# Kernel optimization log

Measured on AMD Instinct MI355X. Metric: run time of the kernel, lower is better.

The kernel has to match this reference:

```python
import jax, jax.numpy as jnp
import numpy as np

EMBED_SIZE = 100
HEAD_SIZE = 64
B, T = 4, 4096


def setup_inputs() -> dict:
    key = jax.random.key(0)
    k1, k2, k3, k4 = jax.random.split(key, 4)
    x = jax.random.normal(k1, (B, T, EMBED_SIZE), dtype=jnp.float32)
    Wq = jax.random.normal(k2, (EMBED_SIZE, HEAD_SIZE), dtype=jnp.float32) * 0.1
    Wk = jax.random.normal(k3, (EMBED_SIZE, HEAD_SIZE), dtype=jnp.float32) * 0.1
    Wv = jax.random.normal(k4, (EMBED_SIZE, HEAD_SIZE), dtype=jnp.float32) * 0.1
    return {"x": x, "Wq": Wq, "Wk": Wk, "Wv": Wv}


def reference(x, Wq, Wk, Wv):
    # Projections (bias-free Linear): [B, T, head_size]
    q = x @ Wq
    k = x @ Wk
    v = x @ Wv
    scale = HEAD_SIZE ** (-0.5)
    # Scaled scores [B, T, T]
    scores = jnp.einsum("bqd,bkd->bqk", q, k) * scale
    # Faithful to source: tril the scores, then mask entries that equal 0 to -inf
    masked = jnp.tril(scores)
    masked = jnp.where(masked == 0, -jnp.inf, masked)
    attn = jax.nn.softmax(masked, axis=-1)
    out = jnp.einsum("bqk,bkd->bqd", attn, v)  # [B, T, head_size]
    return out
```

## Files before the change

kernel.cpp:

```cpp
#include <hip/hip_runtime.h>
#include <hip/hip_bf16.h>
#include <stdint.h>

#define NB 4
#define NT 4096
#define NE 100
#define ND 64

typedef __attribute__((ext_vector_type(8))) short short8;
typedef __attribute__((ext_vector_type(4))) short short4_;
typedef __attribute__((ext_vector_type(4))) float float4_;
typedef unsigned short ushort_t;

__device__ __forceinline__ unsigned short f2bf(float f) {
  union { float f; uint32_t u; } v; v.f = f;
  uint32_t u = v.u;
  u += 0x7fffu + ((u >> 16) & 1u);
  return (unsigned short)(u >> 16);
}

__device__ __forceinline__ float bf2f(short us) {
  union { uint32_t u; float f; } v;
  v.u = ((uint32_t)(unsigned short)us) << 16;
  return v.f;
}

__device__ __forceinline__ float fast_exp2(float x) {
#if __has_builtin(__builtin_amdgcn_exp2f)
  return __builtin_amdgcn_exp2f(x);
#else
  return exp2f(x);
#endif
}

__global__ __launch_bounds__(256) void proj_kernel(
    const float* __restrict__ x, const float* __restrict__ Wq,
    const float* __restrict__ Wk, const float* __restrict__ Wv,
    ushort_t* __restrict__ Qb, ushort_t* __restrict__ Kb,
    ushort_t* __restrict__ Vt) {
  __shared__ __align__(16) float xs[16 * NE];
  __shared__ __align__(16) ushort_t Wl[3][25][64][4];
  ushort_t (*Vl)[72] = (ushort_t(*)[72])xs;

  const int tid = threadIdx.x;
  const int r0  = blockIdx.x * 16;

  {
    const float4_* xsrc = (const float4_*)(x + (size_t)r0 * NE);
    float4_* xdst = (float4_*)xs;
    #pragma unroll
    for (int i = tid; i < 400; i += 256) xdst[i] = xsrc[i];
  }
  {
    const int ch = tid >> 6, d = tid & 63;
    if (ch < 3) {
      const float* Ws = (ch == 0) ? Wq : (ch == 1) ? Wk : Wv;
      #pragma unroll 5
      for (int qd = 0; qd < 25; ++qd) {
        short4_ pk;
        #pragma unroll
        for (int jj = 0; jj < 4; ++jj)
          pk[jj] = (short)f2bf(Ws[(4*qd + jj)*ND + d]);
        *(short4_*)&Wl[ch][qd][d][0] = pk;
      }
    }
  }
  __syncthreads();

  const int wv = tid >> 6, lane = tid & 63;
  float aq[4] = {0,0,0,0}, ak[4] = {0,0,0,0}, av[4] = {0,0,0,0};
  const float* xw = xs + (wv * 4) * NE;

  for (int qd = 0; qd < 25; ++qd) {
    short4_ w4q = *(const short4_*)&Wl[0][qd][lane][0];
    short4_ w4k = *(const short4_*)&Wl[1][qd][lane][0];
    short4_ w4v = *(const short4_*)&Wl[2][qd][lane][0];
    float4_ x0 = *(const float4_*)&xw[0*NE + 4*qd];
    float4_ x1 = *(const float4_*)&xw[1*NE + 4*qd];
    float4_ x2 = *(const float4_*)&xw[2*NE + 4*qd];
    float4_ x3 = *(const float4_*)&xw[3*NE + 4*qd];
    #pragma unroll
    for (int jj = 0; jj < 4; ++jj) {
      float fq = bf2f(w4q[jj]), fk = bf2f(w4k[jj]), fv = bf2f(w4v[jj]);
      aq[0] += x0[jj]*fq; ak[0] += x0[jj]*fk; av[0] += x0[jj]*fv;
      aq[1] += x1[jj]*fq; ak[1] += x1[jj]*fk; av[1] += x1[jj]*fv;
      aq[2] += x2[jj]*fq; ak[2] += x2[jj]*fk; av[2] += x2[jj]*fv;
      aq[3] += x3[jj]*fq; ak[3] += x3[jj]*fk; av[3] += x3[jj]*fv;
    }
  }

  __syncthreads();

  const float QS = 0.125f * 1.44269504088896340736f;
  #pragma unroll
  for (int j = 0; j < 4; ++j) {
    int row = r0 + wv*4 + j;
    Qb[(size_t)row*ND + lane] = f2bf(aq[j] * QS);
    Kb[(size_t)row*ND + lane] = f2bf(ak[j]);
    Vl[wv*4 + j][lane] = f2bf(av[j]);
  }
  __syncthreads();

  if (tid < 128) {
    int d = tid >> 1, halfi = tid & 1;
    short8 pk;
    #pragma unroll
    for (int k2 = 0; k2 < 8; ++k2) pk[k2] = (short)Vl[halfi*8 + k2][d];
    int b = r0 >> 12, tg = (r0 & (NT-1)) + halfi*8;
    *(short8*)(Vt + ((size_t)(b*ND + d))*NT + tg) = pk;
  }
}

__global__ __launch_bounds__(128) void attn_kernel(
    const ushort_t* __restrict__ Qb,
    const ushort_t* __restrict__ Kb,
    const ushort_t* __restrict__ Vt,
    float* __restrict__ out) {
  __shared__ __align__(16) ushort_t Ks[2][64*64];
  __shared__ __align__(16) ushort_t Vs[2][64*64];
  __shared__ __align__(16) ushort_t Pbuf[2][16][72];

  const int tid  = threadIdx.x;
  const int w    = tid >> 6, lane = tid & 63;
  const int qrow = lane & 15, grp = lane >> 4;
  const int blk  = blockIdx.x;
  const int b    = blk >> 6;
  const int pr   = blk & 63;
  const int srow8 = lane >> 3, sc16 = lane & 7;

  const ushort_t* Kbase = Kb + (size_t)b*NT*ND;
  const ushort_t* Vtb   = Vt + (size_t)b*ND*NT;

  for (int half = 0; half < 2; ++half) {
    const int g  = half ? pr : (127 - pr);
    const int q0 = g << 5;
    const int nt = (g >> 1) + 1;
    const int qglob = q0 + 16*w + qrow;

    const ushort_t* Qr = Qb + ((size_t)(b*NT + q0 + 16*w + qrow))*ND + 8*grp;
    const short8 qf0 = *(const short8*)(Qr);
    const short8 qf1 = *(const short8*)(Qr + 32);

    float4_ O0 = {0,0,0,0}, O1 = {0,0,0,0}, O2 = {0,0,0,0}, O3 = {0,0,0,0};
    float m = -1e30f, lsum = 0.f;
    short8 sr[8];

    #pragma unroll
    for (int i = 0; i < 8; ++i) {
      int row = 8*i + srow8;
      sr[i] = (w == 0)
        ? *(const short8*)(Kbase + (size_t)row*ND + sc16*8)
        : *(const short8*)(Vtb + (size_t)row*NT + sc16*8);
    }
    {
      ushort_t* dst = (w == 0) ? Ks[0] : Vs[0];
      #pragma unroll
      for (int i = 0; i < 8; ++i) {
        int row = 8*i + srow8;
        *(short8*)&dst[row*64 + ((sc16 ^ (row & 7)) << 3)] = sr[i];
      }
    }
    __syncthreads();

    for (int t = 0; t < nt; ++t) {
      const int cur = t & 1;
      const int kv0 = t << 6;

      if (t + 1 < nt) {
        const int kn0 = kv0 + 64;
        #pragma unroll
        for (int i = 0; i < 8; ++i) {
          int row = 8*i + srow8;
          sr[i] = (w == 0)
            ? *(const short8*)(Kbase + (size_t)(kn0 + row)*ND + sc16*8)
            : *(const short8*)(Vtb + (size_t)row*NT + kn0 + sc16*8);
        }
      }

      const ushort_t* Kc = Ks[cur];
      const ushort_t* Vc = Vs[cur];

      float4_ s[4];
      #pragma unroll
      for (int st = 0; st < 4; ++st) {
        int row = st*16 + qrow;
        short8 kf0 = *(const short8*)&Kc[row*64 + (((grp    ) ^ (row & 7)) << 3)];
        short8 kf1 = *(const short8*)&Kc[row*64 + (((grp + 4) ^ (row & 7)) << 3)];
        float4_ acc = {0,0,0,0};
        acc = __builtin_amdgcn_mfma_f32_16x16x32_bf16(kf0, qf0, acc, 0,0,0);
        acc = __builtin_amdgcn_mfma_f32_16x16x32_bf16(kf1, qf1, acc, 0,0,0);
        s[st] = acc;
      }

      short8 vf[8];
      #pragma unroll
      for (int j = 0; j < 4; ++j) {
        int row = j*16 + qrow;
        vf[2*j]   = *(const short8*)&Vc[row*64 + (((grp    ) ^ (row & 7)) << 3)];
        vf[2*j+1] = *(const short8*)&Vc[row*64 + (((grp + 4) ^ (row & 7)) << 3)];
      }

      if (t == nt - 1) {
        #pragma unroll
        for (int st = 0; st < 4; ++st)
          #pragma unroll
          for (int r = 0; r < 4; ++r) {
            int kv = kv0 + st*16 + grp*4 + r;
            if (kv > qglob) s[st][r] = -1e30f;
          }
      }

      float pmax = s[0][0];
      #pragma unroll
      for (int st = 0; st < 4; ++st)
        #pragma unroll
        for (int r = 0; r < 4; ++r) pmax = fmaxf(pmax, s[st][r]);
      if (!__all(pmax <= m + 8.0f)) {
        float tm = pmax;
        tm = fmaxf(tm, __shfl_xor(tm, 16));
        tm = fmaxf(tm, __shfl_xor(tm, 32));
        const float mnew  = fmaxf(m, tm);
        const float alpha = fast_exp2(m - mnew);
        m = mnew;
        lsum *= alpha;
        #pragma unroll
        for (int r = 0; r < 4; ++r) {
          float ar = __shfl(alpha, grp*4 + r);
          O0[r] *= ar; O1[r] *= ar; O2[r] *= ar; O3[r] *= ar;
        }
      }

      float psum = 0.f;
      #pragma unroll
      for (int st = 0; st < 4; ++st) {
        short4_ pv;
        #pragma unroll
        for (int r = 0; r < 4; ++r) {
          float p = fast_exp2(s[st][r] - m);
          psum += p;
          pv[r] = (short)f2bf(p);
        }
        *(short4_*)&Pbuf[w][qrow][st*16 + grp*4] = pv;
      }
      psum += __shfl_xor(psum, 16);
      psum += __shfl_xor(psum, 32);
      lsum += psum;

      asm volatile("s_waitcnt lgkmcnt(0)" ::: "memory");

      const short8 pf0 = *(const short8*)&Pbuf[w][qrow][8*grp];
      const short8 pf1 = *(const short8*)&Pbuf[w][qrow][32 + 8*grp];
      O0 = __builtin_amdgcn_mfma_f32_16x16x32_bf16(pf0, vf[0], O0, 0,0,0);
      O0 = __builtin_amdgcn_mfma_f32_16x16x32_bf16(pf1, vf[1], O0, 0,0,0);
      O1 = __builtin_amdgcn_mfma_f32_16x16x32_bf16(pf0, vf[2], O1, 0,0,0);
      O1 = __builtin_amdgcn_mfma_f32_16x16x32_bf16(pf1, vf[3], O1, 0,0,0);
      O2 = __builtin_amdgcn_mfma_f32_16x16x32_bf16(pf0, vf[4], O2, 0,0,0);
      O2 = __builtin_amdgcn_mfma_f32_16x16x32_bf16(pf1, vf[5], O2, 0,0,0);
      O3 = __builtin_amdgcn_mfma_f32_16x16x32_bf16(pf0, vf[6], O3, 0,0,0);
      O3 = __builtin_amdgcn_mfma_f32_16x16x32_bf16(pf1, vf[7], O3, 0,0,0);

      if (t + 1 < nt) {
        ushort_t* dst = (w == 0) ? Ks[cur ^ 1] : Vs[cur ^ 1];
        #pragma unroll
        for (int i = 0; i < 8; ++i) {
          int row = 8*i + srow8;
          *(short8*)&dst[row*64 + ((sc16 ^ (row & 7)) << 3)] = sr[i];
        }
      }
      __syncthreads();
    }

    float* orow = out + ((size_t)(b*NT + q0 + 16*w)) * ND;
    #pragma unroll
    for (int r = 0; r < 4; ++r) {
      float ls  = __shfl(lsum, grp*4 + r);
      float inv = 1.f / ls;
      int qr = grp*4 + r;
      orow[qr*ND + 0*16 + qrow] = O0[r]*inv;
      orow[qr*ND + 1*16 + qrow] = O1[r]*inv;
      orow[qr*ND + 2*16 + qrow] = O2[r]*inv;
      orow[qr*ND + 3*16 + qrow] = O3[r]*inv;
    }
  }
}

extern "C" void kernel_launch(void* const* d_in, const int* in_sizes, int n_in,
                              void* d_out, int out_size, void* d_ws, size_t ws_size,
                              hipStream_t stream) {
  const float* x  = (const float*)d_in[0];
  const float* Wq = (const float*)d_in[1];
  const float* Wk = (const float*)d_in[2];
  const float* Wv = (const float*)d_in[3];
  float* out = (float*)d_out;

  ushort_t* Qb = (ushort_t*)d_ws;
  ushort_t* Kb = Qb + (size_t)NB*NT*ND;
  ushort_t* Vt = Kb + (size_t)NB*NT*ND;

  proj_kernel<<<dim3(1024), dim3(256), 0, stream>>>(x, Wq, Wk, Wv, Qb, Kb, Vt);
  attn_kernel<<<dim3(NB*64), dim3(128), 0, stream>>>(Qb, Kb, Vt, out);
}
```

Measured before the change: 144.0 us.

## Split long causal rows across KV blocks with last-block merge

The attention kernel now uses split-KV (flash-decoding style). Each query group is divided into up to four KV chunks according to its causal length, giving 1280 workgroups instead of 256. Partial O, m and l are written to workspace, and the last finishing block, found through an atomic counter, merges them. The projection kernel now handles 64 rows per block and zeroes the counters, with V transposed in its own shared buffer. This targets poor occupancy and the load imbalance of pairing rows, at the cost of partial-result traffic and a serial merge step.

```diff
diff --git a/kernel.cpp b/kernel.cpp
--- a/kernel.cpp
+++ b/kernel.cpp
@@ -37,19 +37,20 @@
     const float* __restrict__ x, const float* __restrict__ Wq,
     const float* __restrict__ Wk, const float* __restrict__ Wv,
     ushort_t* __restrict__ Qb, ushort_t* __restrict__ Kb,
-    ushort_t* __restrict__ Vt) {
-  __shared__ __align__(16) float xs[16 * NE];
+    ushort_t* __restrict__ Vt, int* __restrict__ cnt) {
+  __shared__ __align__(16) float xs[64 * NE];
   __shared__ __align__(16) ushort_t Wl[3][25][64][4];
-  ushort_t (*Vl)[72] = (ushort_t(*)[72])xs;
+  __shared__ __align__(16) ushort_t Vl[64][72];
 
   const int tid = threadIdx.x;
-  const int r0  = blockIdx.x * 16;
+  const int r0  = blockIdx.x * 64;
+
+  if (blockIdx.x == 0) { cnt[tid] = 0; cnt[tid + 256] = 0; }
 
   {
     const float4_* xsrc = (const float4_*)(x + (size_t)r0 * NE);
     float4_* xdst = (float4_*)xs;
-    #pragma unroll
-    for (int i = tid; i < 400; i += 256) xdst[i] = xsrc[i];
+    for (int i = tid; i < 1600; i += 256) xdst[i] = xsrc[i];
   }
   {
     const int ch = tid >> 6, d = tid & 63;
@@ -68,92 +69,210 @@
   __syncthreads();
 
   const int wv = tid >> 6, lane = tid & 63;
-  float aq[4] = {0,0,0,0}, ak[4] = {0,0,0,0}, av[4] = {0,0,0,0};
-  const float* xw = xs + (wv * 4) * NE;
-
-  for (int qd = 0; qd < 25; ++qd) {
-    short4_ w4q = *(const short4_*)&Wl[0][qd][lane][0];
-    short4_ w4k = *(const short4_*)&Wl[1][qd][lane][0];
-    short4_ w4v = *(const short4_*)&Wl[2][qd][lane][0];
-    float4_ x0 = *(const float4_*)&xw[0*NE + 4*qd];
-    float4_ x1 = *(const float4_*)&xw[1*NE + 4*qd];
-    float4_ x2 = *(const float4_*)&xw[2*NE + 4*qd];
-    float4_ x3 = *(const float4_*)&xw[3*NE + 4*qd];
-    #pragma unroll
-    for (int jj = 0; jj < 4; ++jj) {
-      float fq = bf2f(w4q[jj]), fk = bf2f(w4k[jj]), fv = bf2f(w4v[jj]);
-      aq[0] += x0[jj]*fq; ak[0] += x0[jj]*fk; av[0] += x0[jj]*fv;
-      aq[1] += x1[jj]*fq; ak[1] += x1[jj]*fk; av[1] += x1[jj]*fv;
-      aq[2] += x2[jj]*fq; ak[2] += x2[jj]*fk; av[2] += x2[jj]*fv;
-      aq[3] += x3[jj]*fq; ak[3] += x3[jj]*fk; av[3] += x3[jj]*fv;
-    }
-  }
-
+  const float QS = 0.125f * 1.44269504088896340736f;
+
+  for (int it = 0; it < 4; ++it) {
+    float aq[4] = {0,0,0,0}, ak[4] = {0,0,0,0}, av[4] = {0,0,0,0};
+    const float* xw = xs + (it*16 + wv*4) * NE;
+    for (int qd = 0; qd < 25; ++qd) {
+      short4_ w4q = *(const short4_*)&Wl[0][qd][lane][0];
+      short4_ w4k = *(const short4_*)&Wl[1][qd][lane][0];
+      short4_ w4v = *(const short4_*)&Wl[2][qd][lane][0];
+      float4_ x0 = *(const float4_*)&xw[0*NE + 4*qd];
+      float4_ x1 = *(const float4_*)&xw[1*NE + 4*qd];
+      float4_ x2 = *(const float4_*)&xw[2*NE + 4*qd];
+      float4_ x3 = *(const float4_*)&xw[3*NE + 4*qd];
+      #pragma unroll
+      for (int jj = 0; jj < 4; ++jj) {
+        float fq = bf2f(w4q[jj]), fk = bf2f(w4k[jj]), fv = bf2f(w4v[jj]);
+        aq[0] += x0[jj]*fq; ak[0] += x0[jj]*fk; av[0] += x0[jj]*fv;
+        aq[1] += x1[jj]*fq; ak[1] += x1[jj]*fk; av[1] += x1[jj]*fv;
+        aq[2] += x2[jj]*fq; ak[2] += x2[jj]*fk; av[2] += x2[jj]*fv;
+        aq[3] += x3[jj]*fq; ak[3] += x3[jj]*fk; av[3] += x3[jj]*fv;
+      }
+    }
+    #pragma unroll
+    for (int j = 0; j < 4; ++j) {
+      int lrow = it*16 + wv*4 + j;
+      int row  = r0 + lrow;
+      Qb[(size_t)row*ND + lane] = f2bf(aq[j] * QS);
+      Kb[(size_t)row*ND + lane] = f2bf(ak[j]);
+      Vl[lrow][lane] = f2bf(av[j]);
+    }
+  }
   __syncthreads();
 
-  const float QS = 0.125f * 1.44269504088896340736f;
-  #pragma unroll
-  for (int j = 0; j < 4; ++j) {
-    int row = r0 + wv*4 + j;
-    Qb[(size_t)row*ND + lane] = f2bf(aq[j] * QS);
-    Kb[(size_t)row*ND + lane] = f2bf(ak[j]);
-    Vl[wv*4 + j][lane] = f2bf(av[j]);
-  }
-  __syncthreads();
-
-  if (tid < 128) {
-    int d = tid >> 1, halfi = tid & 1;
-    short8 pk;
-    #pragma unroll
-    for (int k2 = 0; k2 < 8; ++k2) pk[k2] = (short)Vl[halfi*8 + k2][d];
-    int b = r0 >> 12, tg = (r0 & (NT-1)) + halfi*8;
-    *(short8*)(Vt + ((size_t)(b*ND + d))*NT + tg) = pk;
+  {
+    const int b = r0 >> 12, r0t = r0 & (NT - 1);
+    for (int i = tid; i < 512; i += 256) {
+      int d = i >> 3, seg = i & 7;
+      short8 pk;
+      #pragma unroll
+      for (int k2 = 0; k2 < 8; ++k2) pk[k2] = (short)Vl[seg*8 + k2][d];
+      *(short8*)(Vt + ((size_t)(b*ND + d))*NT + r0t + seg*8) = pk;
+    }
   }
 }
 
 __global__ __launch_bounds__(128) void attn_kernel(
-    const ushort_t* __restrict__ Qb,
-    const ushort_t* __restrict__ Kb,
-    const ushort_t* __restrict__ Vt,
+    const ushort_t* __restrict__ Qb, const ushort_t* __restrict__ Kb,
+    const ushort_t* __restrict__ Vt, float* __restrict__ part,
+    float* __restrict__ mlbuf, int* __restrict__ cnt,
     float* __restrict__ out) {
   __shared__ __align__(16) ushort_t Ks[2][64*64];
   __shared__ __align__(16) ushort_t Vs[2][64*64];
   __shared__ __align__(16) ushort_t Pbuf[2][16][72];
+  __shared__ int isLast;
 
   const int tid  = threadIdx.x;
   const int w    = tid >> 6, lane = tid & 63;
   const int qrow = lane & 15, grp = lane >> 4;
-  const int blk  = blockIdx.x;
-  const int b    = blk >> 6;
-  const int pr   = blk & 63;
   const int srow8 = lane >> 3, sc16 = lane & 7;
+
+  const int wid = blockIdx.x;
+  const int b   = wid / 320;
+  const int u   = 319 - (wid - b*320);
+  int g, s;
+  if (u < 32)       { g = u;                                s = 0; }
+  else if (u < 96)  { int v = u - 32;              g = 32 + (v >> 1); s = v & 1; }
+  else if (u < 192) { int v = u - 96; int q3 = v/3; g = 64 + q3;      s = v - 3*q3; }
+  else              { int v = u - 192;             g = 96 + (v >> 2); s = v & 3; }
+
+  const int nt = (g >> 1) + 1;
+  const int nw = (g + 32) >> 5;
+  const int t0 = s << 4;
+  const int t1 = min(nt, t0 + 16);
+  const int q0 = g << 5;
+  const int qglob = q0 + 16*w + qrow;
 
   const ushort_t* Kbase = Kb + (size_t)b*NT*ND;
   const ushort_t* Vtb   = Vt + (size_t)b*ND*NT;
 
-  for (int half = 0; half < 2; ++half) {
-    const int g  = half ? pr : (127 - pr);
-    const int q0 = g << 5;
-    const int nt = (g >> 1) + 1;
-    const int qglob = q0 + 16*w + qrow;
-
-    const ushort_t* Qr = Qb + ((size_t)(b*NT + q0 + 16*w + qrow))*ND + 8*grp;
-    const short8 qf0 = *(const short8*)(Qr);
-    const short8 qf1 = *(const short8*)(Qr + 32);
-
-    float4_ O0 = {0,0,0,0}, O1 = {0,0,0,0}, O2 = {0,0,0,0}, O3 = {0,0,0,0};
-    float m = -1e30f, lsum = 0.f;
-    short8 sr[8];
-
+  const ushort_t* Qr = Qb + ((size_t)(b*NT + q0 + 16*w + qrow))*ND + 8*grp;
+  const short8 qf0 = *(const short8*)(Qr);
+  const short8 qf1 = *(const short8*)(Qr + 32);
+
+  float4_ O0 = {0,0,0,0}, O1 = {0,0,0,0}, O2 = {0,0,0,0}, O3 = {0,0,0,0};
+  float m = -1e30f, lsum = 0.f;
+  short8 sr[8];
+
+  {
+    const int kv0 = t0 << 6;
     #pragma unroll
     for (int i = 0; i < 8; ++i) {
       int row = 8*i + srow8;
       sr[i] = (w == 0)
-        ? *(const short8*)(Kbase + (size_t)row*ND + sc16*8)
-        : *(const short8*)(Vtb + (size_t)row*NT + sc16*8);
-    }
-    {
-      ushort_t* dst = (w == 0) ? Ks[0] : Vs[0];
+        ? *(const short8*)(Kbase + (size_t)(kv0 + row)*ND + sc16*8)
+        : *(const short8*)(Vtb + (size_t)row*NT + kv0 + sc16*8);
+    }
+    ushort_t* dst = (w == 0) ? Ks[0] : Vs[0];
+    #pragma unroll
+    for (int i = 0; i < 8; ++i) {
+      int row = 8*i + srow8;
+      *(short8*)&dst[row*64 + ((sc16 ^ (row & 7)) << 3)] = sr[i];
+    }
+  }
+  __syncthreads();
+
+  for (int t = t0; t < t1; ++t) {
+    const int cur = (t - t0) & 1;
+    const int kv0 = t << 6;
+
+    if (t + 1 < t1) {
+      const int kn0 = kv0 + 64;
+      #pragma unroll
+      for (int i = 0; i < 8; ++i) {
+        int row = 8*i + srow8;
+        sr[i] = (w == 0)
+          ? *(const short8*)(Kbase + (size_t)(kn0 + row)*ND + sc16*8)
+          : *(const short8*)(Vtb + (size_t)row*NT + kn0 + sc16*8);
+      }
+    }
+
+    const ushort_t* Kc = Ks[cur];
+    const ushort_t* Vc = Vs[cur];
+
+    float4_ sA[4];
+    #pragma unroll
+    for (int st = 0; st < 4; ++st) {
+      int row = st*16 + qrow;
+      short8 kf0 = *(const short8*)&Kc[row*64 + (((grp    ) ^ (row & 7)) << 3)];
+      short8 kf1 = *(const short8*)&Kc[row*64 + (((grp + 4) ^ (row & 7)) << 3)];
+      float4_ acc = {0,0,0,0};
+      acc = __builtin_amdgcn_mfma_f32_16x16x32_bf16(kf0, qf0, acc, 0,0,0);
+      acc = __builtin_amdgcn_mfma_f32_16x16x32_bf16(kf1, qf1, acc, 0,0,0);
+      sA[st] = acc;
+    }
+
+    short8 vf[8];
+    #pragma unroll
+    for (int j = 0; j < 4; ++j) {
+      int row = j*16 + qrow;
+      vf[2*j]   = *(const short8*)&Vc[row*64 + (((grp    ) ^ (row & 7)) << 3)];
+      vf[2*j+1] = *(const short8*)&Vc[row*64 + (((grp + 4) ^ (row & 7)) << 3)];
+    }
+
+    if (t == nt - 1) {
+      #pragma unroll
+      for (int st = 0; st < 4; ++st)
+        #pragma unroll
+        for (int r = 0; r < 4; ++r) {
+          int kv = kv0 + st*16 + grp*4 + r;
+          if (kv > qglob) sA[st][r] = -1e30f;
+        }
+    }
+
+    float pmax = sA[0][0];
+    #pragma unroll
+    for (int st = 0; st < 4; ++st)
+      #pragma unroll
+      for (int r = 0; r < 4; ++r) pmax = fmaxf(pmax, sA[st][r]);
+    if (!__all(pmax <= m + 8.0f)) {
+      float tm = pmax;
+      tm = fmaxf(tm, __shfl_xor(tm, 16));
+      tm = fmaxf(tm, __shfl_xor(tm, 32));
+      const float mnew  = fmaxf(m, tm);
+      const float alpha = fast_exp2(m - mnew);
+      m = mnew;
+      lsum *= alpha;
+      #pragma unroll
+      for (int r = 0; r < 4; ++r) {
+        float ar = __shfl(alpha, grp*4 + r);
+        O0[r] *= ar; O1[r] *= ar; O2[r] *= ar; O3[r] *= ar;
+      }
+    }
+
+    float psum = 0.f;
+    #pragma unroll
+    for (int st = 0; st < 4; ++st) {
+      short4_ pv;
+      #pragma unroll
+      for (int r = 0; r < 4; ++r) {
+        float p = fast_exp2(sA[st][r] - m);
+        psum += p;
+        pv[r] = (short)f2bf(p);
+      }
+      *(short4_*)&Pbuf[w][qrow][st*16 + grp*4] = pv;
+    }
+    psum += __shfl_xor(psum, 16);
+    psum += __shfl_xor(psum, 32);
+    lsum += psum;
+
+    asm volatile("s_waitcnt lgkmcnt(0)" ::: "memory");
+
+    const short8 pf0 = *(const short8*)&Pbuf[w][qrow][8*grp];
+    const short8 pf1 = *(const short8*)&Pbuf[w][qrow][32 + 8*grp];
+    O0 = __builtin_amdgcn_mfma_f32_16x16x32_bf16(pf0, vf[0], O0, 0,0,0);
+    O0 = __builtin_amdgcn_mfma_f32_16x16x32_bf16(pf1, vf[1], O0, 0,0,0);
+    O1 = __builtin_amdgcn_mfma_f32_16x16x32_bf16(pf0, vf[2], O1, 0,0,0);
+    O1 = __builtin_amdgcn_mfma_f32_16x16x32_bf16(pf1, vf[3], O1, 0,0,0);
+    O2 = __builtin_amdgcn_mfma_f32_16x16x32_bf16(pf0, vf[4], O2, 0,0,0);
+    O2 = __builtin_amdgcn_mfma_f32_16x16x32_bf16(pf1, vf[5], O2, 0,0,0);
+    O3 = __builtin_amdgcn_mfma_f32_16x16x32_bf16(pf0, vf[6], O3, 0,0,0);
+    O3 = __builtin_amdgcn_mfma_f32_16x16x32_bf16(pf1, vf[7], O3, 0,0,0);
+
+    if (t + 1 < t1) {
+      ushort_t* dst = (w == 0) ? Ks[cur ^ 1] : Vs[cur ^ 1];
       #pragma unroll
       for (int i = 0; i < 8; ++i) {
         int row = 8*i + srow8;
@@ -161,125 +280,55 @@
       }
     }
     __syncthreads();
-
-    for (int t = 0; t < nt; ++t) {
-      const int cur = t & 1;
-      const int kv0 = t << 6;
-
-      if (t + 1 < nt) {
-        const int kn0 = kv0 + 64;
-        #pragma unroll
-        for (int i = 0; i < 8; ++i) {
-          int row = 8*i + srow8;
-          sr[i] = (w == 0)
-            ? *(const short8*)(Kbase + (size_t)(kn0 + row)*ND + sc16*8)
-            : *(const short8*)(Vtb + (size_t)row*NT + kn0 + sc16*8);
-        }
-      }
-
-      const ushort_t* Kc = Ks[cur];
-      const ushort_t* Vc = Vs[cur];
-
-      float4_ s[4];
-      #pragma unroll
-      for (int st = 0; st < 4; ++st) {
-        int row = st*16 + qrow;
-        short8 kf0 = *(const short8*)&Kc[row*64 + (((grp    ) ^ (row & 7)) << 3)];
-        short8 kf1 = *(const short8*)&Kc[row*64 + (((grp + 4) ^ (row & 7)) << 3)];
-        float4_ acc = {0,0,0,0};
-        acc = __builtin_amdgcn_mfma_f32_16x16x32_bf16(kf0, qf0, acc, 0,0,0);
-        acc = __builtin_amdgcn_mfma_f32_16x16x32_bf16(kf1, qf1, acc, 0,0,0);
-        s[st] = acc;
-      }
-
-      short8 vf[8];
-      #pragma unroll
-      for (int j = 0; j < 4; ++j) {
-        int row = j*16 + qrow;
-        vf[2*j]   = *(const short8*)&Vc[row*64 + (((grp    ) ^ (row & 7)) << 3)];
-        vf[2*j+1] = *(const short8*)&Vc[row*64 + (((grp + 4) ^ (row & 7)) << 3)];
-      }
-
-      if (t == nt - 1) {
-        #pragma unroll
-        for (int st = 0; st < 4; ++st)
-          #pragma unroll
-          for (int r = 0; r < 4; ++r) {
-            int kv = kv0 + st*16 + grp*4 + r;
-            if (kv > qglob) s[st][r] = -1e30f;
-          }
-      }
-
-      float pmax = s[0][0];
-      #pragma unroll
-      for (int st = 0; st < 4; ++st)
-        #pragma unroll
-        for (int r = 0; r < 4; ++r) pmax = fmaxf(pmax, s[st][r]);
-      if (!__all(pmax <= m + 8.0f)) {
-        float tm = pmax;
-        tm = fmaxf(tm, __shfl_xor(tm, 16));
-        tm = fmaxf(tm, __shfl_xor(tm, 32));
-        const float mnew  = fmaxf(m, tm);
-        const float alpha = fast_exp2(m - mnew);
-        m = mnew;
-        lsum *= alpha;
-        #pragma unroll
-        for (int r = 0; r < 4; ++r) {
-          float ar = __shfl(alpha, grp*4 + r);
-          O0[r] *= ar; O1[r] *= ar; O2[r] *= ar; O3[r] *= ar;
-        }
-      }
-
-      float psum = 0.f;
-      #pragma unroll
-      for (int st = 0; st < 4; ++st) {
-        short4_ pv;
-        #pragma unroll
-        for (int r = 0; r < 4; ++r) {
-          float p = fast_exp2(s[st][r] - m);
-          psum += p;
-          pv[r] = (short)f2bf(p);
-        }
-        *(short4_*)&Pbuf[w][qrow][st*16 + grp*4] = pv;
-      }
-      psum += __shfl_xor(psum, 16);
-      psum += __shfl_xor(psum, 32);
-      lsum += psum;
-
-      asm volatile("s_waitcnt lgkmcnt(0)" ::: "memory");
-
-      const short8 pf0 = *(const short8*)&Pbuf[w][qrow][8*grp];
-      const short8 pf1 = *(const short8*)&Pbuf[w][qrow][32 + 8*grp];
-      O0 = __builtin_amdgcn_mfma_f32_16x16x32_bf16(pf0, vf[0], O0, 0,0,0);
-      O0 = __builtin_amdgcn_mfma_f32_16x16x32_bf16(pf1, vf[1], O0, 0,0,0);
-      O1 = __builtin_amdgcn_mfma_f32_16x16x32_bf16(pf0, vf[2], O1, 0,0,0);
-      O1 = __builtin_amdgcn_mfma_f32_16x16x32_bf16(pf1, vf[3], O1, 0,0,0);
-      O2 = __builtin_amdgcn_mfma_f32_16x16x32_bf16(pf0, vf[4], O2, 0,0,0);
-      O2 = __builtin_amdgcn_mfma_f32_16x16x32_bf16(pf1, vf[5], O2, 0,0,0);
-      O3 = __builtin_amdgcn_mfma_f32_16x16x32_bf16(pf0, vf[6], O3, 0,0,0);
-      O3 = __builtin_amdgcn_mfma_f32_16x16x32_bf16(pf1, vf[7], O3, 0,0,0);
-
-      if (t + 1 < nt) {
-        ushort_t* dst = (w == 0) ? Ks[cur ^ 1] : Vs[cur ^ 1];
-        #pragma unroll
-        for (int i = 0; i < 8; ++i) {
-          int row = 8*i + srow8;
-          *(short8*)&dst[row*64 + ((sc16 ^ (row & 7)) << 3)] = sr[i];
-        }
-      }
-      __syncthreads();
-    }
-
+  }
+
+  if (nw == 1) {
     float* orow = out + ((size_t)(b*NT + q0 + 16*w)) * ND;
     #pragma unroll
     for (int r = 0; r < 4; ++r) {
-      float ls  = __shfl(lsum, grp*4 + r);
-      float inv = 1.f / ls;
+      float inv = 1.f / __shfl(lsum, grp*4 + r);
       int qr = grp*4 + r;
       orow[qr*ND + 0*16 + qrow] = O0[r]*inv;
       orow[qr*ND + 1*16 + qrow] = O1[r]*inv;
       orow[qr*ND + 2*16 + qrow] = O2[r]*inv;
       orow[qr*ND + 3*16 + qrow] = O3[r]*inv;
+    }
+  } else {
+    const int gi = b*128 + g;
+    float* Op  = part  + ((size_t)gi*4 + s)*2048;
+    float* Mlp = mlbuf + ((size_t)gi*4 + s)*64;
+    #pragma unroll
+    for (int r = 0; r < 4; ++r) {
+      int row = 16*w + grp*4 + r;
+      Op[row*64 + 0*16 + qrow] = O0[r];
+      Op[row*64 + 1*16 + qrow] = O1[r];
+      Op[row*64 + 2*16 + qrow] = O2[r];
+      Op[row*64 + 3*16 + qrow] = O3[r];
+    }
+    if (lane < 16) { Mlp[(16*w + lane)*2] = m; Mlp[(16*w + lane)*2 + 1] = lsum; }
+    __syncthreads();
+    if (tid == 0) {
+      __threadfence();
+      int old = atomicAdd(&cnt[gi], 1);
+      isLast = (old == nw - 1) ? 1 : 0;
+    }
+    __syncthreads();
+    if (isLast) {
+      __threadfence();
+      const float* Pp = part  + (size_t)gi*4*2048;
+      const float* Mp = mlbuf + (size_t)gi*4*64;
+      for (int i = tid; i < 2048; i += 128) {
+        int row = i >> 6, d = i & 63;
+        float M = -1e30f;
+        for (int s2 = 0; s2 < nw; ++s2) M = fmaxf(M, Mp[s2*64 + row*2]);
+        float ls = 0.f, o = 0.f;
+        for (int s2 = 0; s2 < nw; ++s2) {
+          float sc = fast_exp2(Mp[s2*64 + row*2] - M);
+          ls += sc * Mp[s2*64 + row*2 + 1];
+          o  += sc * Pp[(size_t)s2*2048 + row*64 + d];
+        }
+        out[((size_t)b*NT + q0 + row)*ND + d] = o / ls;
+      }
     }
   }
 }
@@ -293,10 +342,14 @@
   const float* Wv = (const float*)d_in[3];
   float* out = (float*)d_out;
 
-  ushort_t* Qb = (ushort_t*)d_ws;
-  ushort_t* Kb = Qb + (size_t)NB*NT*ND;
-  ushort_t* Vt = Kb + (size_t)NB*NT*ND;
-
-  proj_kernel<<<dim3(1024), dim3(256), 0, stream>>>(x, Wq, Wk, Wv, Qb, Kb, Vt);
-  attn_kernel<<<dim3(NB*64), dim3(128), 0, stream>>>(Qb, Kb, Vt, out);
-}
+  char* ws = (char*)d_ws;
+  ushort_t* Qb   = (ushort_t*)(ws);
+  ushort_t* Kb   = (ushort_t*)(ws + (2u<<20));
+  ushort_t* Vt   = (ushort_t*)(ws + (4u<<20));
+  float*    part = (float*)(ws + (6u<<20));
+  float*    mlb  = (float*)(ws + (22u<<20));
+  int*      cnt  = (int*)(ws + (22u<<20) + (512u<<10));
+
+  proj_kernel<<<dim3(256), dim3(256), 0, stream>>>(x, Wq, Wk, Wv, Qb, Kb, Vt, cnt);
+  attn_kernel<<<dim3(NB*320), dim3(128), 0, stream>>>(Qb, Kb, Vt, part, mlb, cnt, out);
+}
```

Measured after the change: 213.3 us. +48.1%, slower.

## Split causal KV loop across four wave-pairs per block with LDS softmax merge

Applied to the files above, without the earlier changes.

The attention kernel now runs 512 threads per block. Four wave-pairs each handle every fourth 64-key tile of the causal range, with their own double-buffered K/V staging. Partial outputs and softmax statistics (max, sum) are merged through LDS at the end of each phase. This targets the long serial per-block KV loop on a small 128-thread grid, at the cost of a large dynamic LDS footprint, an extra reduction pass, and a per-call attribute set. Blocks are also remapped so each XCD serves a single batch, and the projection kernel processes 64 rows per block instead of 16.

```diff
diff --git a/kernel.cpp b/kernel.cpp
--- a/kernel.cpp
+++ b/kernel.cpp
@@ -38,18 +38,17 @@
     const float* __restrict__ Wk, const float* __restrict__ Wv,
     ushort_t* __restrict__ Qb, ushort_t* __restrict__ Kb,
     ushort_t* __restrict__ Vt) {
-  __shared__ __align__(16) float xs[16 * NE];
+  __shared__ __align__(16) float xs[64 * NE];
   __shared__ __align__(16) ushort_t Wl[3][25][64][4];
-  ushort_t (*Vl)[72] = (ushort_t(*)[72])xs;
+  __shared__ __align__(16) ushort_t Vl[64][72];
 
   const int tid = threadIdx.x;
-  const int r0  = blockIdx.x * 16;
+  const int r0  = blockIdx.x * 64;
 
   {
     const float4_* xsrc = (const float4_*)(x + (size_t)r0 * NE);
     float4_* xdst = (float4_*)xs;
-    #pragma unroll
-    for (int i = tid; i < 400; i += 256) xdst[i] = xsrc[i];
+    for (int i = tid; i < 1600; i += 256) xdst[i] = xsrc[i];
   }
   {
     const int ch = tid >> 6, d = tid & 63;
@@ -68,76 +67,86 @@
   __syncthreads();
 
   const int wv = tid >> 6, lane = tid & 63;
-  float aq[4] = {0,0,0,0}, ak[4] = {0,0,0,0}, av[4] = {0,0,0,0};
-  const float* xw = xs + (wv * 4) * NE;
-
-  for (int qd = 0; qd < 25; ++qd) {
-    short4_ w4q = *(const short4_*)&Wl[0][qd][lane][0];
-    short4_ w4k = *(const short4_*)&Wl[1][qd][lane][0];
-    short4_ w4v = *(const short4_*)&Wl[2][qd][lane][0];
-    float4_ x0 = *(const float4_*)&xw[0*NE + 4*qd];
-    float4_ x1 = *(const float4_*)&xw[1*NE + 4*qd];
-    float4_ x2 = *(const float4_*)&xw[2*NE + 4*qd];
-    float4_ x3 = *(const float4_*)&xw[3*NE + 4*qd];
+  const float QS = 0.125f * 1.44269504088896340736f;
+
+  for (int it = 0; it < 4; ++it) {
+    float aq[4] = {0,0,0,0}, ak[4] = {0,0,0,0}, av[4] = {0,0,0,0};
+    const float* xw = xs + (it*16 + wv*4) * NE;
+    for (int qd = 0; qd < 25; ++qd) {
+      short4_ w4q = *(const short4_*)&Wl[0][qd][lane][0];
+      short4_ w4k = *(const short4_*)&Wl[1][qd][lane][0];
+      short4_ w4v = *(const short4_*)&Wl[2][qd][lane][0];
+      float4_ x0 = *(const float4_*)&xw[0*NE + 4*qd];
+      float4_ x1 = *(const float4_*)&xw[1*NE + 4*qd];
+      float4_ x2 = *(const float4_*)&xw[2*NE + 4*qd];
+      float4_ x3 = *(const float4_*)&xw[3*NE + 4*qd];
+      #pragma unroll
+      for (int jj = 0; jj < 4; ++jj) {
+        float fq = bf2f(w4q[jj]), fk = bf2f(w4k[jj]), fv = bf2f(w4v[jj]);
+        aq[0] += x0[jj]*fq; ak[0] += x0[jj]*fk; av[0] += x0[jj]*fv;
+        aq[1] += x1[jj]*fq; ak[1] += x1[jj]*fk; av[1] += x1[jj]*fv;
+        aq[2] += x2[jj]*fq; ak[2] += x2[jj]*fk; av[2] += x2[jj]*fv;
+        aq[3] += x3[jj]*fq; ak[3] += x3[jj]*fk; av[3] += x3[jj]*fv;
+      }
+    }
     #pragma unroll
-    for (int jj = 0; jj < 4; ++jj) {
-      float fq = bf2f(w4q[jj]), fk = bf2f(w4k[jj]), fv = bf2f(w4v[jj]);
-      aq[0] += x0[jj]*fq; ak[0] += x0[jj]*fk; av[0] += x0[jj]*fv;
-      aq[1] += x1[jj]*fq; ak[1] += x1[jj]*fk; av[1] += x1[jj]*fv;
-      aq[2] += x2[jj]*fq; ak[2] += x2[jj]*fk; av[2] += x2[jj]*fv;
-      aq[3] += x3[jj]*fq; ak[3] += x3[jj]*fk; av[3] += x3[jj]*fv;
-    }
-  }
-
+    for (int j = 0; j < 4; ++j) {
+      int lrow = it*16 + wv*4 + j;
+      int row  = r0 + lrow;
+      Qb[(size_t)row*ND + lane] = f2bf(aq[j] * QS);
+      Kb[(size_t)row*ND + lane] = f2bf(ak[j]);
+      Vl[lrow][lane] = f2bf(av[j]);
+    }
+  }
   __syncthreads();
 
-  const float QS = 0.125f * 1.44269504088896340736f;
-  #pragma unroll
-  for (int j = 0; j < 4; ++j) {
-    int row = r0 + wv*4 + j;
-    Qb[(size_t)row*ND + lane] = f2bf(aq[j] * QS);
-    Kb[(size_t)row*ND + lane] = f2bf(ak[j]);
-    Vl[wv*4 + j][lane] = f2bf(av[j]);
-  }
-  __syncthreads();
-
-  if (tid < 128) {
-    int d = tid >> 1, halfi = tid & 1;
-    short8 pk;
-    #pragma unroll
-    for (int k2 = 0; k2 < 8; ++k2) pk[k2] = (short)Vl[halfi*8 + k2][d];
-    int b = r0 >> 12, tg = (r0 & (NT-1)) + halfi*8;
-    *(short8*)(Vt + ((size_t)(b*ND + d))*NT + tg) = pk;
-  }
-}
-
-__global__ __launch_bounds__(128) void attn_kernel(
-    const ushort_t* __restrict__ Qb,
-    const ushort_t* __restrict__ Kb,
-    const ushort_t* __restrict__ Vt,
-    float* __restrict__ out) {
-  __shared__ __align__(16) ushort_t Ks[2][64*64];
-  __shared__ __align__(16) ushort_t Vs[2][64*64];
-  __shared__ __align__(16) ushort_t Pbuf[2][16][72];
+  {
+    const int b = r0 >> 12, r0t = r0 & (NT - 1);
+    for (int i = tid; i < 512; i += 256) {
+      int d = i >> 3, seg = i & 7;
+      short8 pk;
+      #pragma unroll
+      for (int k2 = 0; k2 < 8; ++k2) pk[k2] = (short)Vl[seg*8 + k2][d];
+      *(short8*)(Vt + ((size_t)(b*ND + d))*NT + r0t + seg*8) = pk;
+    }
+  }
+}
+
+__global__ __launch_bounds__(512) void attn_kernel(
+    const ushort_t* __restrict__ Qb, const ushort_t* __restrict__ Kb,
+    const ushort_t* __restrict__ Vt, float* __restrict__ out) {
+  extern __shared__ __align__(16) char arena[];
+  ushort_t* KsB = (ushort_t*)arena;
+  ushort_t* VsB = KsB + 4*2*4096;
+  ushort_t* PbB = VsB + 4*2*4096;
+  float*    Om  = (float*)arena;
+  float*    Ml  = (float*)(arena + 131072);
 
   const int tid  = threadIdx.x;
   const int w    = tid >> 6, lane = tid & 63;
+  const int pp   = w >> 1, h = w & 1;
   const int qrow = lane & 15, grp = lane >> 4;
-  const int blk  = blockIdx.x;
-  const int b    = blk >> 6;
-  const int pr   = blk & 63;
   const int srow8 = lane >> 3, sc16 = lane & 7;
+
+  const int blk = blockIdx.x;
+  const int xcd = blk & 7;
+  const int b   = xcd >> 1;
+  const int p   = ((blk >> 3) << 1) | (xcd & 1);
 
   const ushort_t* Kbase = Kb + (size_t)b*NT*ND;
   const ushort_t* Vtb   = Vt + (size_t)b*ND*NT;
 
-  for (int half = 0; half < 2; ++half) {
-    const int g  = half ? pr : (127 - pr);
+  ushort_t* Ks0 = KsB + pp*8192;
+  ushort_t* Vs0 = VsB + pp*8192;
+  ushort_t* Pw  = PbB + w*1152;
+
+  for (int phase = 0; phase < 2; ++phase) {
+    const int g  = phase ? p : (127 - p);
     const int q0 = g << 5;
     const int nt = (g >> 1) + 1;
-    const int qglob = q0 + 16*w + qrow;
-
-    const ushort_t* Qr = Qb + ((size_t)(b*NT + q0 + 16*w + qrow))*ND + 8*grp;
+    const int qglob = q0 + h*16 + qrow;
+
+    const ushort_t* Qr = Qb + ((size_t)(b*NT + q0 + h*16 + qrow))*ND + 8*grp;
     const short8 qf0 = *(const short8*)(Qr);
     const short8 qf1 = *(const short8*)(Qr + 32);
 
@@ -145,15 +154,18 @@
     float m = -1e30f, lsum = 0.f;
     short8 sr[8];
 
-    #pragma unroll
-    for (int i = 0; i < 8; ++i) {
-      int row = 8*i + srow8;
-      sr[i] = (w == 0)
-        ? *(const short8*)(Kbase + (size_t)row*ND + sc16*8)
-        : *(const short8*)(Vtb + (size_t)row*NT + sc16*8);
-    }
-    {
-      ushort_t* dst = (w == 0) ? Ks[0] : Vs[0];
+    const int maxIter = (nt + 3) >> 2;
+
+    if (pp < nt) {
+      const int kv0 = pp << 6;
+      #pragma unroll
+      for (int i = 0; i < 8; ++i) {
+        int row = 8*i + srow8;
+        sr[i] = (h == 0)
+          ? *(const short8*)(Kbase + (size_t)(kv0 + row)*ND + sc16*8)
+          : *(const short8*)(Vtb + (size_t)row*NT + kv0 + sc16*8);
+      }
+      ushort_t* dst = (h == 0) ? Ks0 : Vs0;
       #pragma unroll
       for (int i = 0; i < 8; ++i) {
         int row = 8*i + srow8;
@@ -162,105 +174,110 @@
     }
     __syncthreads();
 
-    for (int t = 0; t < nt; ++t) {
-      const int cur = t & 1;
-      const int kv0 = t << 6;
-
-      if (t + 1 < nt) {
-        const int kn0 = kv0 + 64;
+    for (int it = 0; it < maxIter; ++it) {
+      const int t    = pp + (it << 2);
+      const int buf  = it & 1;
+      const bool act = (t < nt);
+      const bool hasNext = act && (t + 4 < nt);
+
+      if (hasNext) {
+        const int kn0 = (t + 4) << 6;
         #pragma unroll
         for (int i = 0; i < 8; ++i) {
           int row = 8*i + srow8;
-          sr[i] = (w == 0)
+          sr[i] = (h == 0)
             ? *(const short8*)(Kbase + (size_t)(kn0 + row)*ND + sc16*8)
             : *(const short8*)(Vtb + (size_t)row*NT + kn0 + sc16*8);
         }
       }
 
-      const ushort_t* Kc = Ks[cur];
-      const ushort_t* Vc = Vs[cur];
-
-      float4_ s[4];
-      #pragma unroll
-      for (int st = 0; st < 4; ++st) {
-        int row = st*16 + qrow;
-        short8 kf0 = *(const short8*)&Kc[row*64 + (((grp    ) ^ (row & 7)) << 3)];
-        short8 kf1 = *(const short8*)&Kc[row*64 + (((grp + 4) ^ (row & 7)) << 3)];
-        float4_ acc = {0,0,0,0};
-        acc = __builtin_amdgcn_mfma_f32_16x16x32_bf16(kf0, qf0, acc, 0,0,0);
-        acc = __builtin_amdgcn_mfma_f32_16x16x32_bf16(kf1, qf1, acc, 0,0,0);
-        s[st] = acc;
-      }
-
-      short8 vf[8];
-      #pragma unroll
-      for (int j = 0; j < 4; ++j) {
-        int row = j*16 + qrow;
-        vf[2*j]   = *(const short8*)&Vc[row*64 + (((grp    ) ^ (row & 7)) << 3)];
-        vf[2*j+1] = *(const short8*)&Vc[row*64 + (((grp + 4) ^ (row & 7)) << 3)];
-      }
-
-      if (t == nt - 1) {
+      if (act) {
+        const int kv0 = t << 6;
+        const ushort_t* Kc = Ks0 + buf*4096;
+        const ushort_t* Vc = Vs0 + buf*4096;
+
+        float4_ sA[4];
+        #pragma unroll
+        for (int st = 0; st < 4; ++st) {
+          int row = st*16 + qrow;
+          short8 kf0 = *(const short8*)&Kc[row*64 + (((grp    ) ^ (row & 7)) << 3)];
+          short8 kf1 = *(const short8*)&Kc[row*64 + (((grp + 4) ^ (row & 7)) << 3)];
+          float4_ acc = {0,0,0,0};
+          acc = __builtin_amdgcn_mfma_f32_16x16x32_bf16(kf0, qf0, acc, 0,0,0);
+          acc = __builtin_amdgcn_mfma_f32_16x16x32_bf16(kf1, qf1, acc, 0,0,0);
+          sA[st] = acc;
+        }
+
+        short8 vf[8];
+        #pragma unroll
+        for (int j = 0; j < 4; ++j) {
+          int row = j*16 + qrow;
+          vf[2*j]   = *(const short8*)&Vc[row*64 + (((grp    ) ^ (row & 7)) << 3)];
+          vf[2*j+1] = *(const short8*)&Vc[row*64 + (((grp + 4) ^ (row & 7)) << 3)];
+        }
+
+        if (t == nt - 1) {
+          #pragma unroll
+          for (int st = 0; st < 4; ++st)
+            #pragma unroll
+            for (int r = 0; r < 4; ++r) {
+              int kv = kv0 + st*16 + grp*4 + r;
+              if (kv > qglob) sA[st][r] = -1e30f;
+            }
+        }
+
+        float pmax = sA[0][0];
         #pragma unroll
         for (int st = 0; st < 4; ++st)
           #pragma unroll
+          for (int r = 0; r < 4; ++r) pmax = fmaxf(pmax, sA[st][r]);
+        if (!__all(pmax <= m + 8.0f)) {
+          float tm = pmax;
+          tm = fmaxf(tm, __shfl_xor(tm, 16));
+          tm = fmaxf(tm, __shfl_xor(tm, 32));
+          const float mnew  = fmaxf(m, tm);
+          const float alpha = fast_exp2(m - mnew);
+          m = mnew;
+          lsum *= alpha;
+          #pragma unroll
           for (int r = 0; r < 4; ++r) {
-            int kv = kv0 + st*16 + grp*4 + r;
-            if (kv > qglob) s[st][r] = -1e30f;
+            float ar = __shfl(alpha, grp*4 + r);
+            O0[r] *= ar; O1[r] *= ar; O2[r] *= ar; O3[r] *= ar;
           }
-      }
-
-      float pmax = s[0][0];
-      #pragma unroll
-      for (int st = 0; st < 4; ++st)
-        #pragma unroll
-        for (int r = 0; r < 4; ++r) pmax = fmaxf(pmax, s[st][r]);
-      if (!__all(pmax <= m + 8.0f)) {
-        float tm = pmax;
-        tm = fmaxf(tm, __shfl_xor(tm, 16));
-        tm = fmaxf(tm, __shfl_xor(tm, 32));
-        const float mnew  = fmaxf(m, tm);
-        const float alpha = fast_exp2(m - mnew);
-        m = mnew;
-        lsum *= alpha;
-        #pragma unroll
-        for (int r = 0; r < 4; ++r) {
-          float ar = __shfl(alpha, grp*4 + r);
-          O0[r] *= ar; O1[r] *= ar; O2[r] *= ar; O3[r] *= ar;
-        }
-      }
-
-      float psum = 0.f;
-      #pragma unroll
-      for (int st = 0; st < 4; ++st) {
-        short4_ pv;
-        #pragma unroll
-        for (int r = 0; r < 4; ++r) {
-          float p = fast_exp2(s[st][r] - m);
-          psum += p;
-          pv[r] = (short)f2bf(p);
-        }
-        *(short4_*)&Pbuf[w][qrow][st*16 + grp*4] = pv;
-      }
-      psum += __shfl_xor(psum, 16);
-      psum += __shfl_xor(psum, 32);
-      lsum += psum;
-
-      asm volatile("s_waitcnt lgkmcnt(0)" ::: "memory");
-
-      const short8 pf0 = *(const short8*)&Pbuf[w][qrow][8*grp];
-      const short8 pf1 = *(const short8*)&Pbuf[w][qrow][32 + 8*grp];
-      O0 = __builtin_amdgcn_mfma_f32_16x16x32_bf16(pf0, vf[0], O0, 0,0,0);
-      O0 = __builtin_amdgcn_mfma_f32_16x16x32_bf16(pf1, vf[1], O0, 0,0,0);
-      O1 = __builtin_amdgcn_mfma_f32_16x16x32_bf16(pf0, vf[2], O1, 0,0,0);
-      O1 = __builtin_amdgcn_mfma_f32_16x16x32_bf16(pf1, vf[3], O1, 0,0,0);
-      O2 = __builtin_amdgcn_mfma_f32_16x16x32_bf16(pf0, vf[4], O2, 0,0,0);
-      O2 = __builtin_amdgcn_mfma_f32_16x16x32_bf16(pf1, vf[5], O2, 0,0,0);
-      O3 = __builtin_amdgcn_mfma_f32_16x16x32_bf16(pf0, vf[6], O3, 0,0,0);
-      O3 = __builtin_amdgcn_mfma_f32_16x16x32_bf16(pf1, vf[7], O3, 0,0,0);
-
-      if (t + 1 < nt) {
-        ushort_t* dst = (w == 0) ? Ks[cur ^ 1] : Vs[cur ^ 1];
+        }
+
+        float psum = 0.f;
+        #pragma unroll
+        for (int st = 0; st < 4; ++st) {
+          short4_ pv;
+          #pragma unroll
+          for (int r = 0; r < 4; ++r) {
+            float pe = fast_exp2(sA[st][r] - m);
+            psum += pe;
+            pv[r] = (short)f2bf(pe);
+          }
+          *(short4_*)&Pw[qrow*72 + st*16 + grp*4] = pv;
+        }
+        psum += __shfl_xor(psum, 16);
+        psum += __shfl_xor(psum, 32);
+        lsum += psum;
+
+        asm volatile("s_waitcnt lgkmcnt(0)" ::: "memory");
+
+        const short8 pf0 = *(const short8*)&Pw[qrow*72 + 8*grp];
+        const short8 pf1 = *(const short8*)&Pw[qrow*72 + 32 + 8*grp];
+        O0 = __builtin_amdgcn_mfma_f32_16x16x32_bf16(pf0, vf[0], O0, 0,0,0);
+        O0 = __builtin_amdgcn_mfma_f32_16x16x32_bf16(pf1, vf[1], O0, 0,0,0);
+        O1 = __builtin_amdgcn_mfma_f32_16x16x32_bf16(pf0, vf[2], O1, 0,0,0);
+        O1 = __builtin_amdgcn_mfma_f32_16x16x32_bf16(pf1, vf[3], O1, 0,0,0);
+        O2 = __builtin_amdgcn_mfma_f32_16x16x32_bf16(pf0, vf[4], O2, 0,0,0);
+        O2 = __builtin_amdgcn_mfma_f32_16x16x32_bf16(pf1, vf[5], O2, 0,0,0);
+        O3 = __builtin_amdgcn_mfma_f32_16x16x32_bf16(pf0, vf[6], O3, 0,0,0);
+        O3 = __builtin_amdgcn_mfma_f32_16x16x32_bf16(pf1, vf[7], O3, 0,0,0);
+      }
+
+      if (hasNext) {
+        ushort_t* dst = ((h == 0) ? Ks0 : Vs0) + (buf ^ 1)*4096;
         #pragma unroll
         for (int i = 0; i < 8; ++i) {
           int row = 8*i + srow8;
@@ -270,17 +287,38 @@
       __syncthreads();
     }
 
-    float* orow = out + ((size_t)(b*NT + q0 + 16*w)) * ND;
     #pragma unroll
     for (int r = 0; r < 4; ++r) {
-      float ls  = __shfl(lsum, grp*4 + r);
-      float inv = 1.f / ls;
-      int qr = grp*4 + r;
-      orow[qr*ND + 0*16 + qrow] = O0[r]*inv;
-      orow[qr*ND + 1*16 + qrow] = O1[r]*inv;
-      orow[qr*ND + 2*16 + qrow] = O2[r]*inv;
-      orow[qr*ND + 3*16 + qrow] = O3[r]*inv;
-    }
+      int row = grp*4 + r;
+      Om[w*1024 + row*64 + 0*16 + qrow] = O0[r];
+      Om[w*1024 + row*64 + 1*16 + qrow] = O1[r];
+      Om[w*1024 + row*64 + 2*16 + qrow] = O2[r];
+      Om[w*1024 + row*64 + 3*16 + qrow] = O3[r];
+    }
+    if (lane < 16) {
+      Ml[(w*16 + lane)*2]     = m;
+      Ml[(w*16 + lane)*2 + 1] = lsum;
+    }
+    __syncthreads();
+
+    for (int i = tid; i < 2048; i += 512) {
+      int row = i >> 6, d = i & 63;
+      int hh = row >> 4, r16 = row & 15;
+      float M = -3e30f;
+      #pragma unroll
+      for (int p2 = 0; p2 < 4; ++p2)
+        M = fmaxf(M, Ml[((2*p2 + hh)*16 + r16)*2]);
+      float ls = 0.f, os = 0.f;
+      #pragma unroll
+      for (int p2 = 0; p2 < 4; ++p2) {
+        int w2 = 2*p2 + hh;
+        float sc = fast_exp2(Ml[(w2*16 + r16)*2] - M);
+        ls += sc * Ml[(w2*16 + r16)*2 + 1];
+        os += sc * Om[w2*1024 + r16*64 + d];
+      }
+      out[((size_t)b*NT + q0 + row)*ND + d] = os / ls;
+    }
+    __syncthreads();
   }
 }
 
@@ -297,6 +335,12 @@
   ushort_t* Kb = Qb + (size_t)NB*NT*ND;
   ushort_t* Vt = Kb + (size_t)NB*NT*ND;
 
-  proj_kernel<<<dim3(1024), dim3(256), 0, stream>>>(x, Wq, Wk, Wv, Qb, Kb, Vt);
-  attn_kernel<<<dim3(NB*64), dim3(128), 0, stream>>>(Qb, Kb, Vt, out);
-}
+  const int ldsBytes = (4*2*4096 + 4*2*4096 + 8*16*72) * 2;
+  static bool attrSet = false;
+  (void)attrSet;
+  hipFuncSetAttribute((const void*)attn_kernel,
+                      hipFuncAttributeMaxDynamicSharedMemorySize, ldsBytes);
+
+  proj_kernel<<<dim3(256), dim3(256), 0, stream>>>(x, Wq, Wk, Wv, Qb, Kb, Vt);
+  attn_kernel<<<dim3(256), dim3(512), ldsBytes, stream>>>(Qb, Kb, Vt, out);
+}
```

Result: faster. 124.9 us (-13.3%).
